# Performance work log

Measured on AMD Instinct MI355X. Metric: run time of the kernel, lower is better.

The kernel has to match this reference:

```python
import jax, jax.numpy as jnp
import numpy as np

N = 100000      # nodes
E = 1600000     # edges
F_IN = 512      # num_node_features
HID = 128       # hidden_dim (GCN2Conv channels)
C = 64          # num_classes
L = 8           # n_layers
ALPHA = 0.1
THETA = 0.5


def setup_inputs() -> dict:
    key = jax.random.key(0)
    ks = jax.random.split(key, 7)
    x = jax.random.normal(ks[0], (N, F_IN), jnp.float32)
    edge_index = jax.random.randint(ks[1], (2, E), 0, N, dtype=jnp.int64)
    # fcs[0]: Linear(F_IN, HID); stored as [in, out] so forward is x @ w + b
    w_in = jax.random.normal(ks[2], (F_IN, HID), jnp.float32) / np.sqrt(F_IN)
    b_in = jnp.zeros((HID,), jnp.float32)
    # one shared [H, H] weight per GCN2Conv layer (shared_weights=True)
    conv_w = jax.random.normal(ks[3], (L, HID, HID), jnp.float32) / np.sqrt(HID)
    # fcs[-1]: Linear(HID, C)
    w_out = jax.random.normal(ks[4], (HID, C), jnp.float32) / np.sqrt(HID)
    b_out = jnp.zeros((C,), jnp.float32)
    return dict(x=x, edge_index=edge_index, w_in=w_in, b_in=b_in,
                conv_w=conv_w, w_out=w_out, b_out=b_out)


def _gcn_norm(edge_index, num_nodes):
    # PyG gcn_norm with add_self_loops=True, edge_weight=1
    loops = jnp.arange(num_nodes, dtype=edge_index.dtype)
    src = jnp.concatenate([edge_index[0], loops])
    dst = jnp.concatenate([edge_index[1], loops])
    deg = jax.ops.segment_sum(jnp.ones_like(dst, jnp.float32), dst,
                              num_segments=num_nodes)
    dinv = jnp.where(deg > 0, jax.lax.rsqrt(jnp.maximum(deg, 1e-12)), 0.0)
    norm = dinv[src] * dinv[dst]  # [E + N]
    return src, dst, norm


def reference(x, edge_index, w_in, b_in, conv_w, w_out, b_out):
    src, dst, norm = _gcn_norm(edge_index, N)
    h = x @ w_in + b_in          # fcs[0]; [N, HID]
    h0 = h                       # initial residual
    for l in range(L):
        beta = float(np.log(THETA / (l + 1) + 1.0))
        # sparse neighbor aggregation: out[i] = sum_e norm[e] * h[src[e]]
        agg = jax.ops.segment_sum(h[src] * norm[:, None], dst, num_segments=N)
        s = (1.0 - ALPHA) * agg + ALPHA * h0           # initial residual mix
        h = jax.nn.elu((1.0 - beta) * s + beta * (s @ conv_w[l]))  # identity mapping
        # dropout omitted (eval mode / training=False)
    logits = h @ w_out + b_out   # fcs[-1]
    return jax.nn.log_softmax(logits, axis=-1)
```

## Files before the change

kernel.cpp:

```cpp
#include <hip/hip_runtime.h>
#include <math.h>

#define N_NODES 100000
#define N_EDGES 1600000
#define F_IN    512
#define HID     128
#define NCLS    64
#define NLAYERS 8
#define NT      (N_NODES / 16)
#define NSCANB  ((N_NODES + 255) / 256)

typedef __attribute__((ext_vector_type(8))) short short8;
typedef __attribute__((ext_vector_type(4))) float float4v;

__device__ inline unsigned short f2bf(float f) {
    unsigned int u = __float_as_uint(f);
    unsigned int r = u + 0x7fffu + ((u >> 16) & 1u);
    return (unsigned short)(r >> 16);
}
__device__ inline float bf2f(unsigned short h) {
    return __uint_as_float(((unsigned int)h) << 16);
}
__device__ inline uint4 pack8(const unsigned short* v) {
    uint4 u;
    u.x = (unsigned)v[0] | ((unsigned)v[1] << 16);
    u.y = (unsigned)v[2] | ((unsigned)v[3] << 16);
    u.z = (unsigned)v[4] | ((unsigned)v[5] << 16);
    u.w = (unsigned)v[6] | ((unsigned)v[7] << 16);
    return u;
}
__device__ inline void bf8_fma(float* a, uint4 u, float v) {
    a[0] += v * __uint_as_float(u.x << 16);
    a[1] += v * __uint_as_float(u.x & 0xffff0000u);
    a[2] += v * __uint_as_float(u.y << 16);
    a[3] += v * __uint_as_float(u.y & 0xffff0000u);
    a[4] += v * __uint_as_float(u.z << 16);
    a[5] += v * __uint_as_float(u.z & 0xffff0000u);
    a[6] += v * __uint_as_float(u.w << 16);
    a[7] += v * __uint_as_float(u.w & 0xffff0000u);
}
__device__ inline void split_into(short8& ahi, short8& alo, int j, float f) {
    unsigned short h = f2bf(f);
    ahi[j] = (short)h;
    alo[j] = (short)f2bf(f - bf2f(h));
}


__global__ __launch_bounds__(256) void cnt_init(int* __restrict__ cnt) {
    int i = blockIdx.x * 256 + threadIdx.x;
    if (i < N_NODES) cnt[i] = 0;
}
__global__ __launch_bounds__(256) void cnt_count(const int* __restrict__ dst,
                                                 int* __restrict__ cnt) {
    int e = blockIdx.x * 256 + threadIdx.x;
    if (e < N_EDGES) atomicAdd(&cnt[dst[e]], 1);
}
__global__ __launch_bounds__(256) void make_dinv(const int* __restrict__ cnt,
                                                 float* __restrict__ dinv) {
    int i = blockIdx.x * 256 + threadIdx.x;
    if (i < N_NODES) dinv[i] = rsqrtf((float)(cnt[i] + 1));
}
__global__ __launch_bounds__(256) void scan_block(const int* __restrict__ cnt,
                                                  int* __restrict__ partial,
                                                  int* __restrict__ bsum) {
    __shared__ int tmp[256];
    int t = threadIdx.x, i = blockIdx.x * 256 + t;
    int v = (i < N_NODES) ? cnt[i] : 0;
    tmp[t] = v;
    __syncthreads();
#pragma unroll
    for (int off = 1; off < 256; off <<= 1) {
        int add = (t >= off) ? tmp[t - off] : 0;
        __syncthreads();
        tmp[t] += add;
        __syncthreads();
    }
    if (i < N_NODES) partial[i] = tmp[t];
    if (t == 255) bsum[blockIdx.x] = tmp[255];
}
__global__ void scan_bsum(int* __restrict__ bsum) {
    if (threadIdx.x == 0 && blockIdx.x == 0) {
        int acc = 0;
        for (int i = 0; i < NSCANB; i++) { int v = bsum[i]; bsum[i] = acc; acc += v; }
    }
}
__global__ __launch_bounds__(256) void finalize_rowptr(const int* __restrict__ cnt,
                                                       const int* __restrict__ partial,
                                                       const int* __restrict__ bsum,
                                                       int* __restrict__ row_ptr,
                                                       int* __restrict__ cursor) {
    int i = blockIdx.x * 256 + threadIdx.x;
    if (i < N_NODES) {
        int ex = partial[i] - cnt[i] + bsum[blockIdx.x];
        row_ptr[i] = ex;
        cursor[i]  = ex;
        if (i == N_NODES - 1) row_ptr[N_NODES] = ex + cnt[i];
    }
}
__global__ __launch_bounds__(256) void scatter_edges(const int* __restrict__ srcI,
                                                     const int* __restrict__ dstI,
                                                     const float* __restrict__ dinv,
                                                     int* __restrict__ cursor,
                                                     int2* __restrict__ rec) {
    int e = blockIdx.x * 256 + threadIdx.x;
    if (e < N_EDGES) {
        int s = srcI[e], d = dstI[e];
        int pos = atomicAdd(&cursor[d], 1);
        rec[pos] = make_int2(s, __float_as_int(dinv[s] * dinv[d]));
    }
}

__global__ __launch_bounds__(64) void conv_win(const float* __restrict__ w,
                                               unsigned short* __restrict__ wip) {
    int nt = blockIdx.x >> 4;
    int c  = blockIdx.x & 15;
    int lane = threadIdx.x;
    int n  = nt * 16 + (lane & 15);
    int kb = c * 32 + (lane >> 4) * 8;
    unsigned short hi[8], lo[8];
#pragma unroll
    for (int j = 0; j < 8; j++) {
        float v = w[(size_t)(kb + j) * HID + n];
        hi[j] = f2bf(v);
        lo[j] = f2bf(v - bf2f(hi[j]));
    }
    size_t base = ((size_t)nt * 16 + c) * 1024 + (size_t)lane * 8;
    *(uint4*)&wip[base]       = pack8(hi);
    *(uint4*)&wip[base + 512] = pack8(lo);
}

__global__ __launch_bounds__(64) void conv_wl(const float* __restrict__ cw,
                                              unsigned short* __restrict__ wlp) {
    int l  = blockIdx.x >> 5;
    int nt = (blockIdx.x >> 2) & 7;
    int c  = blockIdx.x & 3;
    int lane = threadIdx.x;
    float beta = logf(0.5f / (float)(l + 1) + 1.0f);
    int n  = nt * 16 + (lane & 15);
    int kb = c * 32 + (lane >> 4) * 8;
    const float* W = cw + (size_t)l * HID * HID;
    unsigned short hi[8], lo[8];
#pragma unroll
    for (int j = 0; j < 8; j++) {
        int k = kb + j;
        float v = beta * W[(size_t)k * HID + n] + ((k == n) ? (1.0f - beta) : 0.0f);
        hi[j] = f2bf(v);
        lo[j] = f2bf(v - bf2f(hi[j]));
    }
    size_t base = (((size_t)l * 8 + nt) * 4 + c) * 1024 + (size_t)lane * 8;
    *(uint4*)&wlp[base]       = pack8(hi);
    *(uint4*)&wlp[base + 512] = pack8(lo);
}

__global__ __launch_bounds__(64) void conv_wout(const float* __restrict__ w,
                                                unsigned short* __restrict__ wop) {
    int nt = blockIdx.x >> 2;
    int c  = blockIdx.x & 3;
    int lane = threadIdx.x;
    int n  = nt * 16 + (lane & 15);
    int kb = c * 32 + (lane >> 4) * 8;
    unsigned short hi[8], lo[8];
#pragma unroll
    for (int j = 0; j < 8; j++) {
        float v = w[(size_t)(kb + j) * NCLS + n];
        hi[j] = f2bf(v);
        lo[j] = f2bf(v - bf2f(hi[j]));
    }
    size_t base = ((size_t)nt * 4 + c) * 1024 + (size_t)lane * 8;
    *(uint4*)&wop[base]       = pack8(hi);
    *(uint4*)&wop[base + 512] = pack8(lo);
}

__global__ __launch_bounds__(256) void in_gemm_mfma(const float* __restrict__ x,
        const unsigned short* __restrict__ wip, const float* __restrict__ bias,
        unsigned short* __restrict__ hb, unsigned short* __restrict__ h0b) {
    __shared__ unsigned short tile[64][136];
    int wave = threadIdx.x >> 6;
    int lane = threadIdx.x & 63;
    int t = blockIdx.x * 4 + wave;
    int m = lane & 15, q = lane >> 4;

    if (t < NT) {
        float4v acc[8];
#pragma unroll
        for (int nt = 0; nt < 8; nt++) acc[nt] = (float4v){0.f, 0.f, 0.f, 0.f};
        const float* xr = x + (size_t)(t * 16 + m) * F_IN + q * 8;
        const short8* wp8 = (const short8*)wip;
        for (int c = 0; c < 16; c++) {
            float4 x0 = *(const float4*)(xr + c * 32);
            float4 x1 = *(const float4*)(xr + c * 32 + 4);
            short8 ahi, alo;
            split_into(ahi, alo, 0, x0.x); split_into(ahi, alo, 1, x0.y);
            split_into(ahi, alo, 2, x0.z); split_into(ahi, alo, 3, x0.w);
            split_into(ahi, alo, 4, x1.x); split_into(ahi, alo, 5, x1.y);
            split_into(ahi, alo, 6, x1.z); split_into(ahi, alo, 7, x1.w);
#pragma unroll
            for (int nt = 0; nt < 8; nt++) {
                short8 bhi = wp8[(size_t)(nt * 16 + c) * 128 + lane];
                short8 blo = wp8[(size_t)(nt * 16 + c) * 128 + 64 + lane];
                acc[nt] = __builtin_amdgcn_mfma_f32_16x16x32_bf16(ahi, bhi, acc[nt], 0, 0, 0);
                acc[nt] = __builtin_amdgcn_mfma_f32_16x16x32_bf16(ahi, blo, acc[nt], 0, 0, 0);
                acc[nt] = __builtin_amdgcn_mfma_f32_16x16x32_bf16(alo, bhi, acc[nt], 0, 0, 0);
            }
        }
#pragma unroll
        for (int nt = 0; nt < 8; nt++) {
            float bb = bias[nt * 16 + m];
#pragma unroll
            for (int r = 0; r < 4; r++)
                tile[wave * 16 + q * 4 + r][nt * 16 + m] = f2bf(acc[nt][r] + bb);
        }
    }
    __syncthreads();

    int nl = threadIdx.x >> 2, part = threadIdx.x & 3;
    int node = blockIdx.x * 64 + nl;
    if (node < N_NODES) {
        uint4* d1 = (uint4*)&hb [(size_t)node * HID + part * 32];
        uint4* d2 = (uint4*)&h0b[(size_t)node * HID + part * 32];
#pragma unroll
        for (int j = 0; j < 4; j++) {
            uint4 u = *(uint4*)&tile[nl][part * 32 + j * 8];
            d1[j] = u; d2[j] = u;
        }
    }
}

__global__ __launch_bounds__(256) void spmm_mix(const int* __restrict__ row_ptr,
        const int2* __restrict__ rec, const float* __restrict__ dinv,
        const unsigned short* __restrict__ hb, const unsigned short* __restrict__ h0b,
        float* __restrict__ sout) {
    int node = blockIdx.x * 4 + (threadIdx.x >> 6);
    int lane = threadIdx.x & 63;
    int quarter = lane >> 4;
    int fl = lane & 15;
    int e0 = row_ptr[node], e1 = row_ptr[node + 1];
    float a[8] = {0.f, 0.f, 0.f, 0.f, 0.f, 0.f, 0.f, 0.f};

    int e = e0 + quarter;
    for (; e + 4 < e1; e += 8) {
        int2 r0 = rec[e];
        int2 r1 = rec[e + 4];
        uint4 u0 = *(const uint4*)(hb + (size_t)r0.x * HID + fl * 8);
        uint4 u1 = *(const uint4*)(hb + (size_t)r1.x * HID + fl * 8);
        bf8_fma(a, u0, __int_as_float(r0.y));
        bf8_fma(a, u1, __int_as_float(r1.y));
    }
    for (; e < e1; e += 4) {
        int2 r0 = rec[e];
        uint4 u0 = *(const uint4*)(hb + (size_t)r0.x * HID + fl * 8);
        bf8_fma(a, u0, __int_as_float(r0.y));
    }
#pragma unroll
    for (int j = 0; j < 8; j++) {
        a[j] += __shfl_xor(a[j], 16);
        a[j] += __shfl_xor(a[j], 32);
    }
    if (quarter == 0) {
        float dd = dinv[node], d2 = dd * dd;
        uint4 hv = *(const uint4*)(hb  + (size_t)node * HID + fl * 8);
        uint4 zv = *(const uint4*)(h0b + (size_t)node * HID + fl * 8);
        float hvf[8], zvf[8];
        hvf[0] = __uint_as_float(hv.x << 16); hvf[1] = __uint_as_float(hv.x & 0xffff0000u);
        hvf[2] = __uint_as_float(hv.y << 16); hvf[3] = __uint_as_float(hv.y & 0xffff0000u);
        hvf[4] = __uint_as_float(hv.z << 16); hvf[5] = __uint_as_float(hv.z & 0xffff0000u);
        hvf[6] = __uint_as_float(hv.w << 16); hvf[7] = __uint_as_float(hv.w & 0xffff0000u);
        zvf[0] = __uint_as_float(zv.x << 16); zvf[1] = __uint_as_float(zv.x & 0xffff0000u);
        zvf[2] = __uint_as_float(zv.y << 16); zvf[3] = __uint_as_float(zv.y & 0xffff0000u);
        zvf[4] = __uint_as_float(zv.z << 16); zvf[5] = __uint_as_float(zv.z & 0xffff0000u);
        zvf[6] = __uint_as_float(zv.w << 16); zvf[7] = __uint_as_float(zv.w & 0xffff0000u);
        float o[8];
#pragma unroll
        for (int j = 0; j < 8; j++)
            o[j] = 0.9f * (a[j] + d2 * hvf[j]) + 0.1f * zvf[j];
        float4* dst = (float4*)(sout + (size_t)node * HID + fl * 8);
        dst[0] = make_float4(o[0], o[1], o[2], o[3]);
        dst[1] = make_float4(o[4], o[5], o[6], o[7]);
    }
}

__global__ __launch_bounds__(256) void layer_gemm_bf(const float* __restrict__ s,
        const unsigned short* __restrict__ wlp, unsigned short* __restrict__ hb) {
    __shared__ unsigned short tile[64][136];
    int wave = threadIdx.x >> 6;
    int lane = threadIdx.x & 63;
    int t = blockIdx.x * 4 + wave;
    int m = lane & 15, q = lane >> 4;

    if (t < NT) {
        float4v acc[8];
#pragma unroll
        for (int nt = 0; nt < 8; nt++) acc[nt] = (float4v){0.f, 0.f, 0.f, 0.f};
        const float* sr = s + (size_t)(t * 16 + m) * HID + q * 8;
        const short8* wp8 = (const short8*)wlp;
#pragma unroll
        for (int c = 0; c < 4; c++) {
            float4 x0 = *(const float4*)(sr + c * 32);
            float4 x1 = *(const float4*)(sr + c * 32 + 4);
            short8 ahi, alo;
            split_into(ahi, alo, 0, x0.x); split_into(ahi, alo, 1, x0.y);
            split_into(ahi, alo, 2, x0.z); split_into(ahi, alo, 3, x0.w);
            split_into(ahi, alo, 4, x1.x); split_into(ahi, alo, 5, x1.y);
            split_into(ahi, alo, 6, x1.z); split_into(ahi, alo, 7, x1.w);
#pragma unroll
            for (int nt = 0; nt < 8; nt++) {
                short8 bhi = wp8[(size_t)(nt * 4 + c) * 128 + lane];
                short8 blo = wp8[(size_t)(nt * 4 + c) * 128 + 64 + lane];
                acc[nt] = __builtin_amdgcn_mfma_f32_16x16x32_bf16(ahi, bhi, acc[nt], 0, 0, 0);
                acc[nt] = __builtin_amdgcn_mfma_f32_16x16x32_bf16(ahi, blo, acc[nt], 0, 0, 0);
                acc[nt] = __builtin_amdgcn_mfma_f32_16x16x32_bf16(alo, bhi, acc[nt], 0, 0, 0);
            }
        }
#pragma unroll
        for (int nt = 0; nt < 8; nt++) {
#pragma unroll
            for (int r = 0; r < 4; r++) {
                float v = acc[nt][r];
                v = (v > 0.f) ? v : (expf(v) - 1.0f);
                tile[wave * 16 + q * 4 + r][nt * 16 + m] = f2bf(v);
            }
        }
    }
    __syncthreads();

    int nl = threadIdx.x >> 2, part = threadIdx.x & 3;
    int node = blockIdx.x * 64 + nl;
    if (node < N_NODES) {
        uint4* d1 = (uint4*)&hb[(size_t)node * HID + part * 32];
#pragma unroll
        for (int j = 0; j < 4; j++) d1[j] = *(uint4*)&tile[nl][part * 32 + j * 8];
    }
}

__global__ __launch_bounds__(256) void layer_gemm_last(const float* __restrict__ s,
        const unsigned short* __restrict__ wlp, float* __restrict__ hf) {
    int wave = threadIdx.x >> 6;
    int lane = threadIdx.x & 63;
    int t = blockIdx.x * 4 + wave;
    int m = lane & 15, q = lane >> 4;
    if (t >= NT) return;

    float4v acc[8];
#pragma unroll
    for (int nt = 0; nt < 8; nt++) acc[nt] = (float4v){0.f, 0.f, 0.f, 0.f};
    const float* sr = s + (size_t)(t * 16 + m) * HID + q * 8;
    const short8* wp8 = (const short8*)wlp;
#pragma unroll
    for (int c = 0; c < 4; c++) {
        float4 x0 = *(const float4*)(sr + c * 32);
        float4 x1 = *(const float4*)(sr + c * 32 + 4);
        short8 ahi, alo;
        split_into(ahi, alo, 0, x0.x); split_into(ahi, alo, 1, x0.y);
        split_into(ahi, alo, 2, x0.z); split_into(ahi, alo, 3, x0.w);
        split_into(ahi, alo, 4, x1.x); split_into(ahi, alo, 5, x1.y);
        split_into(ahi, alo, 6, x1.z); split_into(ahi, alo, 7, x1.w);
#pragma unroll
        for (int nt = 0; nt < 8; nt++) {
            short8 bhi = wp8[(size_t)(nt * 4 + c) * 128 + lane];
            short8 blo = wp8[(size_t)(nt * 4 + c) * 128 + 64 + lane];
            acc[nt] = __builtin_amdgcn_mfma_f32_16x16x32_bf16(ahi, bhi, acc[nt], 0, 0, 0);
            acc[nt] = __builtin_amdgcn_mfma_f32_16x16x32_bf16(ahi, blo, acc[nt], 0, 0, 0);
            acc[nt] = __builtin_amdgcn_mfma_f32_16x16x32_bf16(alo, bhi, acc[nt], 0, 0, 0);
        }
    }
#pragma unroll
    for (int nt = 0; nt < 8; nt++) {
#pragma unroll
        for (int r = 0; r < 4; r++) {
            float v = acc[nt][r];
            v = (v > 0.f) ? v : (expf(v) - 1.0f);
            hf[(size_t)(t * 16 + q * 4 + r) * HID + nt * 16 + m] = v;
        }
    }
}

__global__ __launch_bounds__(256) void out_gemm(const float* __restrict__ hf,
        const unsigned short* __restrict__ wop, const float* __restrict__ bias,
        float* __restrict__ out) {
    int wave = threadIdx.x >> 6;
    int lane = threadIdx.x & 63;
    int t = blockIdx.x * 4 + wave;
    int m = lane & 15, q = lane >> 4;
    if (t >= NT) return;

    float4v acc[4];
#pragma unroll
    for (int nt = 0; nt < 4; nt++) acc[nt] = (float4v){0.f, 0.f, 0.f, 0.f};
    const float* hr = hf + (size_t)(t * 16 + m) * HID + q * 8;
    const short8* wp8 = (const short8*)wop;
#pragma unroll
    for (int c = 0; c < 4; c++) {
        float4 x0 = *(const float4*)(hr + c * 32);
        float4 x1 = *(const float4*)(hr + c * 32 + 4);
        short8 ahi, alo;
        split_into(ahi, alo, 0, x0.x); split_into(ahi, alo, 1, x0.y);
        split_into(ahi, alo, 2, x0.z); split_into(ahi, alo, 3, x0.w);
        split_into(ahi, alo, 4, x1.x); split_into(ahi, alo, 5, x1.y);
        split_into(ahi, alo, 6, x1.z); split_into(ahi, alo, 7, x1.w);
#pragma unroll
        for (int nt = 0; nt < 4; nt++) {
            short8 bhi = wp8[(size_t)(nt * 4 + c) * 128 + lane];
            short8 blo = wp8[(size_t)(nt * 4 + c) * 128 + 64 + lane];
            acc[nt] = __builtin_amdgcn_mfma_f32_16x16x32_bf16(ahi, bhi, acc[nt], 0, 0, 0);
            acc[nt] = __builtin_amdgcn_mfma_f32_16x16x32_bf16(ahi, blo, acc[nt], 0, 0, 0);
            acc[nt] = __builtin_amdgcn_mfma_f32_16x16x32_bf16(alo, bhi, acc[nt], 0, 0, 0);
        }
    }
    float bn[4];
#pragma unroll
    for (int nt = 0; nt < 4; nt++) bn[nt] = bias[nt * 16 + m];
#pragma unroll
    for (int r = 0; r < 4; r++) {
        float v0 = acc[0][r] + bn[0], v1 = acc[1][r] + bn[1];
        float v2 = acc[2][r] + bn[2], v3 = acc[3][r] + bn[3];
        float mx = fmaxf(fmaxf(v0, v1), fmaxf(v2, v3));
#pragma unroll
        for (int msk = 1; msk < 16; msk <<= 1) mx = fmaxf(mx, __shfl_xor(mx, msk));
        float ssum = expf(v0 - mx) + expf(v1 - mx) + expf(v2 - mx) + expf(v3 - mx);
#pragma unroll
        for (int msk = 1; msk < 16; msk <<= 1) ssum += __shfl_xor(ssum, msk);
        float lg = mx + logf(ssum);
        size_t base = (size_t)(t * 16 + q * 4 + r) * NCLS + m;
        out[base]      = v0 - lg;
        out[base + 16] = v1 - lg;
        out[base + 32] = v2 - lg;
        out[base + 48] = v3 - lg;
    }
}


extern "C" void kernel_launch(void* const* d_in, const int* in_sizes, int n_in,
                              void* d_out, int out_size, void* d_ws, size_t ws_size,
                              hipStream_t stream) {
    const float* x      = (const float*)d_in[0];
    const int*   ei     = (const int*)  d_in[1];
    const float* w_in   = (const float*)d_in[2];
    const float* b_in   = (const float*)d_in[3];
    const float* conv_w = (const float*)d_in[4];
    const float* w_out  = (const float*)d_in[5];
    const float* b_out  = (const float*)d_in[6];
    float* out = (float*)d_out;

    const int* srcI = ei;
    const int* dstI = ei + N_EDGES;

    char* ws = (char*)d_ws;
    float* dinv    = (float*)(ws + 0x000000);
    int*   cnt     = (int*)  (ws + 0x080000);
    int*   partial = (int*)  (ws + 0x100000);
    int*   bsum    = (int*)  (ws + 0x180000);
    int*   row_ptr = (int*)  (ws + 0x190000);
    int*   cursor  = (int*)  (ws + 0x200000);
    int2*  rec     = (int2*) (ws + 0x280000);
    unsigned short* wip = (unsigned short*)(ws + 0xF00000);
    unsigned short* wlp = (unsigned short*)(ws + 0xF40000);
    unsigned short* wop = (unsigned short*)(ws + 0xFC0000);
    unsigned short* hb  = (unsigned short*)(ws + 0x1000000);
    unsigned short* h0b = hb + (size_t)N_NODES * HID;
    float* sbuf = (float*)(h0b + (size_t)N_NODES * HID);
    float* hf   = sbuf + (size_t)N_NODES * HID;

    int gN = (N_NODES + 255) / 256;
    int gE = (N_EDGES + 255) / 256;
    int gT = (NT + 3) / 4;

    cnt_init<<<gN, 256, 0, stream>>>(cnt);
    cnt_count<<<gE, 256, 0, stream>>>(dstI, cnt);
    make_dinv<<<gN, 256, 0, stream>>>(cnt, dinv);
    scan_block<<<NSCANB, 256, 0, stream>>>(cnt, partial, bsum);
    scan_bsum<<<1, 64, 0, stream>>>(bsum);
    finalize_rowptr<<<NSCANB, 256, 0, stream>>>(cnt, partial, bsum, row_ptr, cursor);
    scatter_edges<<<gE, 256, 0, stream>>>(srcI, dstI, dinv, cursor, rec);

    conv_win<<<128, 64, 0, stream>>>(w_in, wip);
    conv_wl<<<256, 64, 0, stream>>>(conv_w, wlp);
    conv_wout<<<16, 64, 0, stream>>>(w_out, wop);

    in_gemm_mfma<<<gT, 256, 0, stream>>>(x, wip, b_in, hb, h0b);

    for (int l = 0; l < NLAYERS; l++) {
        spmm_mix<<<N_NODES / 4, 256, 0, stream>>>(row_ptr, rec, dinv, hb, h0b, sbuf);
        const unsigned short* wl = wlp + (size_t)l * 32768;
        if (l < NLAYERS - 1)
            layer_gemm_bf<<<gT, 256, 0, stream>>>(sbuf, wl, hb);
        else
            layer_gemm_last<<<gT, 256, 0, stream>>>(sbuf, wl, hf);
    }

    out_gemm<<<gT, 256, 0, stream>>>(hf, wop, b_out, out);
}
```

Measured before the change: 1.398 ms.

## Stage packed weights through LDS with register prefetch; unroll SpMM gather by four

The packed weight layouts are reordered so each K-chunk is contiguous. The input and layer GEMMs then cooperatively load each chunk into shared memory, double-buffered through registers, instead of every wave reading weights from global memory. The SpMM loop gains a 4-way unrolled gather stage to put more independent loads in flight. The cost is extra LDS use, two barriers per chunk, and clamped tile indices so out-of-range waves still take part in the barriers.

```diff
diff --git a/kernel.cpp b/kernel.cpp
--- a/kernel.cpp
+++ b/kernel.cpp
@@ -124,7 +124,7 @@
         hi[j] = f2bf(v);
         lo[j] = f2bf(v - bf2f(hi[j]));
     }
-    size_t base = ((size_t)nt * 16 + c) * 1024 + (size_t)lane * 8;
+    size_t base = ((size_t)c * 8 + nt) * 1024 + (size_t)lane * 8;
     *(uint4*)&wip[base]       = pack8(hi);
     *(uint4*)&wip[base + 512] = pack8(lo);
 }
@@ -147,7 +147,7 @@
         hi[j] = f2bf(v);
         lo[j] = f2bf(v - bf2f(hi[j]));
     }
-    size_t base = (((size_t)l * 8 + nt) * 4 + c) * 1024 + (size_t)lane * 8;
+    size_t base = (size_t)l * 32768 + ((size_t)c * 8 + nt) * 1024 + (size_t)lane * 8;
     *(uint4*)&wlp[base]       = pack8(hi);
     *(uint4*)&wlp[base + 512] = pack8(lo);
 }
@@ -174,35 +174,52 @@
 __global__ __launch_bounds__(256) void in_gemm_mfma(const float* __restrict__ x,
         const unsigned short* __restrict__ wip, const float* __restrict__ bias,
         unsigned short* __restrict__ hb, unsigned short* __restrict__ h0b) {
+    __shared__ unsigned short wlds[8192];
     __shared__ unsigned short tile[64][136];
-    int wave = threadIdx.x >> 6;
-    int lane = threadIdx.x & 63;
+    int tid = threadIdx.x;
+    int wave = tid >> 6, lane = tid & 63;
     int t = blockIdx.x * 4 + wave;
     int m = lane & 15, q = lane >> 4;
+    int tc = (t < NT) ? t : (NT - 1);
+
+    const uint4* wg = (const uint4*)wip;
+    uint4 pf0 = wg[tid];
+    uint4 pf1 = wg[tid + 256];
+    uint4 pf2 = wg[tid + 512];
+    uint4 pf3 = wg[tid + 768];
+
+    float4v acc[8];
+#pragma unroll
+    for (int nt = 0; nt < 8; nt++) acc[nt] = (float4v){0.f, 0.f, 0.f, 0.f};
+    const float* xr = x + (size_t)(tc * 16 + m) * F_IN + q * 8;
+    uint4* wl4 = (uint4*)wlds;
+
+    for (int c = 0; c < 16; c++) {
+        wl4[tid] = pf0; wl4[tid + 256] = pf1; wl4[tid + 512] = pf2; wl4[tid + 768] = pf3;
+        __syncthreads();
+        if (c < 15) {
+            const uint4* wn = wg + (size_t)(c + 1) * 1024;
+            pf0 = wn[tid]; pf1 = wn[tid + 256]; pf2 = wn[tid + 512]; pf3 = wn[tid + 768];
+        }
+        float4 x0 = *(const float4*)(xr + c * 32);
+        float4 x1 = *(const float4*)(xr + c * 32 + 4);
+        short8 ahi, alo;
+        split_into(ahi, alo, 0, x0.x); split_into(ahi, alo, 1, x0.y);
+        split_into(ahi, alo, 2, x0.z); split_into(ahi, alo, 3, x0.w);
+        split_into(ahi, alo, 4, x1.x); split_into(ahi, alo, 5, x1.y);
+        split_into(ahi, alo, 6, x1.z); split_into(ahi, alo, 7, x1.w);
+#pragma unroll
+        for (int nt = 0; nt < 8; nt++) {
+            short8 bhi = *(short8*)&wlds[nt * 1024 + lane * 8];
+            short8 blo = *(short8*)&wlds[nt * 1024 + 512 + lane * 8];
+            acc[nt] = __builtin_amdgcn_mfma_f32_16x16x32_bf16(ahi, bhi, acc[nt], 0, 0, 0);
+            acc[nt] = __builtin_amdgcn_mfma_f32_16x16x32_bf16(ahi, blo, acc[nt], 0, 0, 0);
+            acc[nt] = __builtin_amdgcn_mfma_f32_16x16x32_bf16(alo, bhi, acc[nt], 0, 0, 0);
+        }
+        __syncthreads();
+    }
 
     if (t < NT) {
-        float4v acc[8];
-#pragma unroll
-        for (int nt = 0; nt < 8; nt++) acc[nt] = (float4v){0.f, 0.f, 0.f, 0.f};
-        const float* xr = x + (size_t)(t * 16 + m) * F_IN + q * 8;
-        const short8* wp8 = (const short8*)wip;
-        for (int c = 0; c < 16; c++) {
-            float4 x0 = *(const float4*)(xr + c * 32);
-            float4 x1 = *(const float4*)(xr + c * 32 + 4);
-            short8 ahi, alo;
-            split_into(ahi, alo, 0, x0.x); split_into(ahi, alo, 1, x0.y);
-            split_into(ahi, alo, 2, x0.z); split_into(ahi, alo, 3, x0.w);
-            split_into(ahi, alo, 4, x1.x); split_into(ahi, alo, 5, x1.y);
-            split_into(ahi, alo, 6, x1.z); split_into(ahi, alo, 7, x1.w);
-#pragma unroll
-            for (int nt = 0; nt < 8; nt++) {
-                short8 bhi = wp8[(size_t)(nt * 16 + c) * 128 + lane];
-                short8 blo = wp8[(size_t)(nt * 16 + c) * 128 + 64 + lane];
-                acc[nt] = __builtin_amdgcn_mfma_f32_16x16x32_bf16(ahi, bhi, acc[nt], 0, 0, 0);
-                acc[nt] = __builtin_amdgcn_mfma_f32_16x16x32_bf16(ahi, blo, acc[nt], 0, 0, 0);
-                acc[nt] = __builtin_amdgcn_mfma_f32_16x16x32_bf16(alo, bhi, acc[nt], 0, 0, 0);
-            }
-        }
 #pragma unroll
         for (int nt = 0; nt < 8; nt++) {
             float bb = bias[nt * 16 + m];
@@ -213,7 +230,7 @@
     }
     __syncthreads();
 
-    int nl = threadIdx.x >> 2, part = threadIdx.x & 3;
+    int nl = tid >> 2, part = tid & 3;
     int node = blockIdx.x * 64 + nl;
     if (node < N_NODES) {
         uint4* d1 = (uint4*)&hb [(size_t)node * HID + part * 32];
@@ -238,6 +255,20 @@
     float a[8] = {0.f, 0.f, 0.f, 0.f, 0.f, 0.f, 0.f, 0.f};
 
     int e = e0 + quarter;
+    for (; e + 12 < e1; e += 16) {
+        int2 r0 = rec[e];
+        int2 r1 = rec[e + 4];
+        int2 r2 = rec[e + 8];
+        int2 r3 = rec[e + 12];
+        uint4 u0 = *(const uint4*)(hb + (size_t)r0.x * HID + fl * 8);
+        uint4 u1 = *(const uint4*)(hb + (size_t)r1.x * HID + fl * 8);
+        uint4 u2 = *(const uint4*)(hb + (size_t)r2.x * HID + fl * 8);
+        uint4 u3 = *(const uint4*)(hb + (size_t)r3.x * HID + fl * 8);
+        bf8_fma(a, u0, __int_as_float(r0.y));
+        bf8_fma(a, u1, __int_as_float(r1.y));
+        bf8_fma(a, u2, __int_as_float(r2.y));
+        bf8_fma(a, u3, __int_as_float(r3.y));
+    }
     for (; e + 4 < e1; e += 8) {
         int2 r0 = rec[e];
         int2 r1 = rec[e + 4];
@@ -281,36 +312,53 @@
 
 __global__ __launch_bounds__(256) void layer_gemm_bf(const float* __restrict__ s,
         const unsigned short* __restrict__ wlp, unsigned short* __restrict__ hb) {
+    __shared__ unsigned short wlds[8192];
     __shared__ unsigned short tile[64][136];
-    int wave = threadIdx.x >> 6;
-    int lane = threadIdx.x & 63;
+    int tid = threadIdx.x;
+    int wave = tid >> 6, lane = tid & 63;
     int t = blockIdx.x * 4 + wave;
     int m = lane & 15, q = lane >> 4;
+    int tc = (t < NT) ? t : (NT - 1);
+
+    const uint4* wg = (const uint4*)wlp;
+    uint4 pf0 = wg[tid];
+    uint4 pf1 = wg[tid + 256];
+    uint4 pf2 = wg[tid + 512];
+    uint4 pf3 = wg[tid + 768];
+
+    float4v acc[8];
+#pragma unroll
+    for (int nt = 0; nt < 8; nt++) acc[nt] = (float4v){0.f, 0.f, 0.f, 0.f};
+    const float* sr = s + (size_t)(tc * 16 + m) * HID + q * 8;
+    uint4* wl4 = (uint4*)wlds;
+
+#pragma unroll
+    for (int c = 0; c < 4; c++) {
+        wl4[tid] = pf0; wl4[tid + 256] = pf1; wl4[tid + 512] = pf2; wl4[tid + 768] = pf3;
+        __syncthreads();
+        if (c < 3) {
+            const uint4* wn = wg + (size_t)(c + 1) * 1024;
+            pf0 = wn[tid]; pf1 = wn[tid + 256]; pf2 = wn[tid + 512]; pf3 = wn[tid + 768];
+        }
+        float4 x0 = *(const float4*)(sr + c * 32);
+        float4 x1 = *(const float4*)(sr + c * 32 + 4);
+        short8 ahi, alo;
+        split_into(ahi, alo, 0, x0.x); split_into(ahi, alo, 1, x0.y);
+        split_into(ahi, alo, 2, x0.z); split_into(ahi, alo, 3, x0.w);
+        split_into(ahi, alo, 4, x1.x); split_into(ahi, alo, 5, x1.y);
+        split_into(ahi, alo, 6, x1.z); split_into(ahi, alo, 7, x1.w);
+#pragma unroll
+        for (int nt = 0; nt < 8; nt++) {
+            short8 bhi = *(short8*)&wlds[nt * 1024 + lane * 8];
+            short8 blo = *(short8*)&wlds[nt * 1024 + 512 + lane * 8];
+            acc[nt] = __builtin_amdgcn_mfma_f32_16x16x32_bf16(ahi, bhi, acc[nt], 0, 0, 0);
+            acc[nt] = __builtin_amdgcn_mfma_f32_16x16x32_bf16(ahi, blo, acc[nt], 0, 0, 0);
+            acc[nt] = __builtin_amdgcn_mfma_f32_16x16x32_bf16(alo, bhi, acc[nt], 0, 0, 0);
+        }
+        __syncthreads();
+    }
 
     if (t < NT) {
-        float4v acc[8];
-#pragma unroll
-        for (int nt = 0; nt < 8; nt++) acc[nt] = (float4v){0.f, 0.f, 0.f, 0.f};
-        const float* sr = s + (size_t)(t * 16 + m) * HID + q * 8;
-        const short8* wp8 = (const short8*)wlp;
-#pragma unroll
-        for (int c = 0; c < 4; c++) {
-            float4 x0 = *(const float4*)(sr + c * 32);
-            float4 x1 = *(const float4*)(sr + c * 32 + 4);
-            short8 ahi, alo;
-            split_into(ahi, alo, 0, x0.x); split_into(ahi, alo, 1, x0.y);
-            split_into(ahi, alo, 2, x0.z); split_into(ahi, alo, 3, x0.w);
-            split_into(ahi, alo, 4, x1.x); split_into(ahi, alo, 5, x1.y);
-            split_into(ahi, alo, 6, x1.z); split_into(ahi, alo, 7, x1.w);
-#pragma unroll
-            for (int nt = 0; nt < 8; nt++) {
-                short8 bhi = wp8[(size_t)(nt * 4 + c) * 128 + lane];
-                short8 blo = wp8[(size_t)(nt * 4 + c) * 128 + 64 + lane];
-                acc[nt] = __builtin_amdgcn_mfma_f32_16x16x32_bf16(ahi, bhi, acc[nt], 0, 0, 0);
-                acc[nt] = __builtin_amdgcn_mfma_f32_16x16x32_bf16(ahi, blo, acc[nt], 0, 0, 0);
-                acc[nt] = __builtin_amdgcn_mfma_f32_16x16x32_bf16(alo, bhi, acc[nt], 0, 0, 0);
-            }
-        }
 #pragma unroll
         for (int nt = 0; nt < 8; nt++) {
 #pragma unroll
@@ -323,7 +371,7 @@
     }
     __syncthreads();
 
-    int nl = threadIdx.x >> 2, part = threadIdx.x & 3;
+    int nl = tid >> 2, part = tid & 3;
     int node = blockIdx.x * 64 + nl;
     if (node < N_NODES) {
         uint4* d1 = (uint4*)&hb[(size_t)node * HID + part * 32];
@@ -356,8 +404,8 @@
         split_into(ahi, alo, 6, x1.z); split_into(ahi, alo, 7, x1.w);
 #pragma unroll
         for (int nt = 0; nt < 8; nt++) {
-            short8 bhi = wp8[(size_t)(nt * 4 + c) * 128 + lane];
-            short8 blo = wp8[(size_t)(nt * 4 + c) * 128 + 64 + lane];
+            short8 bhi = wp8[(size_t)(c * 8 + nt) * 128 + lane];
+            short8 blo = wp8[(size_t)(c * 8 + nt) * 128 + 64 + lane];
             acc[nt] = __builtin_amdgcn_mfma_f32_16x16x32_bf16(ahi, bhi, acc[nt], 0, 0, 0);
             acc[nt] = __builtin_amdgcn_mfma_f32_16x16x32_bf16(ahi, blo, acc[nt], 0, 0, 0);
             acc[nt] = __builtin_amdgcn_mfma_f32_16x16x32_bf16(alo, bhi, acc[nt], 0, 0, 0);
```

After: 1.270 ms. 9.2% less time.
